# Kernel optimization log

Hardware: AMD Instinct MI355X
Metric: run time of the kernel (lower is better)

## Reference

```python
import jax, jax.numpy as jnp
import numpy as np

BN_EPS = 1e-3  # Keras BatchNormalization default epsilon
K = 7          # kernel_size


def setup_inputs() -> dict:
    key = jax.random.key(0)
    ks = jax.random.split(key, 5)
    B, L, C, F = 128, 512, 128, 128
    L_out = L - K + 1  # 506, valid padding, stride 1
    x = jax.random.normal(ks[0], (B, L, C), dtype=jnp.float32)
    # LocallyConnected1D unshared weights: (L_out, K*C, F), lecun_normal ~ N(0, 1/fan_in)
    kernel = jax.random.normal(ks[1], (L_out, K * C, F), dtype=jnp.float32) * (1.0 / np.sqrt(K * C))
    bias = jnp.zeros((L_out, F), dtype=jnp.float32)
    gamma = jnp.ones((F,), dtype=jnp.float32)
    beta = jnp.zeros((F,), dtype=jnp.float32)
    moving_mean = jax.random.normal(ks[2], (F,), dtype=jnp.float32) * 0.1
    moving_var = jax.random.uniform(ks[3], (F,), dtype=jnp.float32, minval=0.5, maxval=1.5)
    return {"x": x, "kernel": kernel, "bias": bias, "gamma": gamma,
            "beta": beta, "moving_mean": moving_mean, "moving_var": moving_var}


def _local_block(x, kernel, bias, gamma, beta, moving_mean, moving_var):
    B, L, C = x.shape
    L_out = L - K + 1
    F = kernel.shape[-1]
    # Patch extraction: idx[l, k] = l + k -> patches (B, L_out, K, C)
    idx = jnp.arange(L_out)[:, None] + jnp.arange(K)[None, :]
    patches = x[:, idx, :]                                  # (B, L_out, K, C)
    w = kernel.reshape(L_out, K, C, F)                      # unshared per-position weights
    y = jnp.einsum('blkc,lkcf->blf', patches, w) + bias     # (B, L_out, F)
    # BatchNorm (inference, axis=-1) fused with affine
    inv = gamma * jax.lax.rsqrt(moving_var + BN_EPS)
    y = y * inv + (beta - moving_mean * inv)
    return jax.nn.relu(y)


def reference(x, kernel, bias, gamma, beta, moving_mean, moving_var):
    return _local_block(x, kernel, bias, gamma, beta, moving_mean, moving_var)
```

## Files before the change

kernel.cpp:

```cpp
#include <hip/hip_runtime.h>
#include <hip/hip_bf16.h>

#define LO 506
#define LL 512
#define CC 128
#define FF 128
#define KC 896
#define BK 32
#define NK 28
#define XS 40
#define WS 40

typedef __attribute__((ext_vector_type(8))) short short8;
typedef __attribute__((ext_vector_type(4))) float floatx4;
typedef __attribute__((ext_vector_type(4))) unsigned int uintx4;
typedef unsigned short ushort_t;

static __device__ __forceinline__ unsigned int pk2(float a, float b) {
    __hip_bfloat16 ha = __float2bfloat16(a);
    __hip_bfloat16 hb = __float2bfloat16(b);
    unsigned short ua, ub;
    __builtin_memcpy(&ua, &ha, 2);
    __builtin_memcpy(&ub, &hb, 2);
    return (unsigned int)ua | ((unsigned int)ub << 16);
}

__global__ __launch_bounds__(512, 4)
void local_block_kernel(const float* __restrict__ x,
                        const float* __restrict__ wg,
                        const float* __restrict__ bias,
                        const float* __restrict__ gamma,
                        const float* __restrict__ beta,
                        const float* __restrict__ mmean,
                        const float* __restrict__ mvar,
                        float* __restrict__ out)
{
    const int bid = blockIdx.x;
    const int xcd = bid & 7;
    const int idx = bid >> 3;
    const int q8  = LO >> 3;
    const int r8  = LO & 7;
    const int l   = (xcd < r8) ? xcd * (q8 + 1) + idx
                               : r8 * (q8 + 1) + (xcd - r8) * q8 + idx;

    const int t    = threadIdx.x;
    const int lane = t & 63;
    const int wave = t >> 6;
    const int q    = lane >> 4;
    const int l16  = lane & 15;
    const int wr   = wave >> 1;
    const int wc   = wave & 1;

    __shared__ __align__(16) ushort_t Xs[2][128 * XS];
    __shared__ __align__(16) ushort_t Wt[2][128 * WS];

    const int am  = t >> 2;
    const int ak0 = (t & 3) * 8;
    const float* aptr = x + (size_t)am * (LL * CC) + l * CC + ak0;

    const int wf  = t & 127;
    const int wk  = (t >> 7) * 8;
    const float* wptr = wg + (size_t)l * (KC * FF) + wf;

    floatx4 acc[2][4] = {};

    floatx4 areg0[2], areg1[2];
    float   wreg0[8], wreg1[8];

#define LOAD_A(AR, KT) { const float* p = aptr + (KT) * BK;                     \
        AR[0] = *(const floatx4*)(p);                                           \
        AR[1] = *(const floatx4*)(p + 4); }

#define LOAD_W(WR, KT) { const float* p = wptr + (size_t)((KT) * BK + wk) * FF; \
        _Pragma("unroll") for (int j = 0; j < 8; ++j)                           \
            WR[j] = __builtin_nontemporal_load(p + j * FF); }

#define STAGE(S, AR, WR) {                                                      \
        uintx4 av = { pk2(AR[0].x, AR[0].y), pk2(AR[0].z, AR[0].w),             \
                      pk2(AR[1].x, AR[1].y), pk2(AR[1].z, AR[1].w) };           \
        *(uintx4*)&Xs[S][am * XS + ak0] = av;                                   \
        uintx4 wv = { pk2(WR[0], WR[1]), pk2(WR[2], WR[3]),                     \
                      pk2(WR[4], WR[5]), pk2(WR[6], WR[7]) };                   \
        *(uintx4*)&Wt[S][wf * WS + wk] = wv; }

#define BAR() {                                                                 \
        asm volatile("s_waitcnt lgkmcnt(0)" ::: "memory");                      \
        __builtin_amdgcn_s_barrier();                                           \
        asm volatile("" ::: "memory"); }

#define COMPUTE(S) {                                                            \
        short8 af[2], bfr[4];                                                   \
        _Pragma("unroll") for (int mi = 0; mi < 2; ++mi)                        \
            af[mi] = *(const short8*)&Xs[S][(wr*32 + mi*16 + l16) * XS + q*8];  \
        _Pragma("unroll") for (int ni = 0; ni < 4; ++ni)                        \
            bfr[ni] = *(const short8*)&Wt[S][(wc*64 + ni*16 + l16) * WS + q*8]; \
        _Pragma("unroll") for (int mi = 0; mi < 2; ++mi)                        \
            _Pragma("unroll") for (int ni = 0; ni < 4; ++ni)                    \
                acc[mi][ni] = __builtin_amdgcn_mfma_f32_16x16x32_bf16(          \
                    af[mi], bfr[ni], acc[mi][ni], 0, 0, 0); }

    LOAD_A(areg0, 0); LOAD_W(wreg0, 0);
    LOAD_A(areg1, 1); LOAD_W(wreg1, 1);

    for (int kt = 0; kt < NK; kt += 2) {
        STAGE(0, areg0, wreg0);
        if (kt + 2 < NK) { LOAD_A(areg0, kt + 2); LOAD_W(wreg0, kt + 2); }
        BAR();
        COMPUTE(0);
        STAGE(1, areg1, wreg1);
        if (kt + 3 < NK) { LOAD_A(areg1, kt + 3); LOAD_W(wreg1, kt + 3); }
        BAR();
        COMPUTE(1);
    }

#pragma unroll
    for (int ni = 0; ni < 4; ++ni) {
        int f = wc*64 + ni*16 + l16;
        float inv = gamma[f] * rsqrtf(mvar[f] + 1e-3f);
        float off = bias[l * FF + f] * inv + beta[f] - mmean[f] * inv;
#pragma unroll
        for (int mi = 0; mi < 2; ++mi) {
#pragma unroll
            for (int rg = 0; rg < 4; ++rg) {
                int b = wr*32 + mi*16 + q*4 + rg;
                float v = acc[mi][ni][rg] * inv + off;
                __builtin_nontemporal_store(fmaxf(v, 0.0f),
                    &out[((size_t)b * LO + l) * FF + f]);
            }
        }
    }
#undef LOAD_A
#undef LOAD_W
#undef STAGE
#undef BAR
#undef COMPUTE
}

extern "C" void kernel_launch(void* const* d_in, const int* in_sizes, int n_in,
                              void* d_out, int out_size, void* d_ws, size_t ws_size,
                              hipStream_t stream) {
    const float* x     = (const float*)d_in[0];
    const float* w     = (const float*)d_in[1];
    const float* bias  = (const float*)d_in[2];
    const float* gamma = (const float*)d_in[3];
    const float* beta  = (const float*)d_in[4];
    const float* mmean = (const float*)d_in[5];
    const float* mvar  = (const float*)d_in[6];
    float* out = (float*)d_out;

    local_block_kernel<<<dim3(LO), dim3(512), 0, stream>>>(
        x, w, bias, gamma, beta, mmean, mvar, out);
}
```

Before: 347.9 us.

## Split batch into two halves per position to double block count

Result: slower. 364.6 us (+4.8%).

```diff
diff --git a/kernel.cpp b/kernel.cpp
--- a/kernel.cpp
+++ b/kernel.cpp
@@ -8,12 +8,14 @@
 #define KC 896
 #define BK 32
 #define NK 28
+#define NB 1012
 #define XS 40
 #define WS 40
 
 typedef __attribute__((ext_vector_type(8))) short short8;
 typedef __attribute__((ext_vector_type(4))) float floatx4;
 typedef __attribute__((ext_vector_type(4))) unsigned int uintx4;
+typedef __attribute__((ext_vector_type(2))) unsigned int uintx2;
 typedef unsigned short ushort_t;
 
 static __device__ __forceinline__ unsigned int pk2(float a, float b) {
@@ -38,47 +40,46 @@
     const int bid = blockIdx.x;
     const int xcd = bid & 7;
     const int idx = bid >> 3;
-    const int q8  = LO >> 3;
-    const int r8  = LO & 7;
-    const int l   = (xcd < r8) ? xcd * (q8 + 1) + idx
+    const int q8  = NB >> 3;
+    const int r8  = NB & 7;
+    const int lin = (xcd < r8) ? xcd * (q8 + 1) + idx
                                : r8 * (q8 + 1) + (xcd - r8) * q8 + idx;
+    const int l     = lin >> 1;
+    const int bhalf = lin & 1;
 
     const int t    = threadIdx.x;
     const int lane = t & 63;
     const int wave = t >> 6;
     const int q    = lane >> 4;
     const int l16  = lane & 15;
-    const int wr   = wave >> 1;
-    const int wc   = wave & 1;
+    const int wrow = wave >> 2;
+    const int wcol = wave & 3;
 
-    __shared__ __align__(16) ushort_t Xs[2][128 * XS];
+    __shared__ __align__(16) ushort_t Xs[2][64 * XS];
     __shared__ __align__(16) ushort_t Wt[2][128 * WS];
 
-    const int am  = t >> 2;
-    const int ak0 = (t & 3) * 8;
-    const float* aptr = x + (size_t)am * (LL * CC) + l * CC + ak0;
+    const int am  = t >> 3;
+    const int ak0 = (t & 7) * 4;
+    const float* aptr = x + (size_t)(bhalf * 64 + am) * (LL * CC) + l * CC + ak0;
 
     const int wf  = t & 127;
     const int wk  = (t >> 7) * 8;
     const float* wptr = wg + (size_t)l * (KC * FF) + wf;
 
-    floatx4 acc[2][4] = {};
+    floatx4 acc[2][2] = {};
 
-    floatx4 areg0[2], areg1[2];
+    floatx4 areg0, areg1;
     float   wreg0[8], wreg1[8];
 
-#define LOAD_A(AR, KT) { const float* p = aptr + (KT) * BK;                     \
-        AR[0] = *(const floatx4*)(p);                                           \
-        AR[1] = *(const floatx4*)(p + 4); }
+#define LOAD_A(AR, KT) { AR = *(const floatx4*)(aptr + (KT) * BK); }
 
 #define LOAD_W(WR, KT) { const float* p = wptr + (size_t)((KT) * BK + wk) * FF; \
         _Pragma("unroll") for (int j = 0; j < 8; ++j)                           \
-            WR[j] = __builtin_nontemporal_load(p + j * FF); }
+            WR[j] = p[j * FF]; }
 
 #define STAGE(S, AR, WR) {                                                      \
-        uintx4 av = { pk2(AR[0].x, AR[0].y), pk2(AR[0].z, AR[0].w),             \
-                      pk2(AR[1].x, AR[1].y), pk2(AR[1].z, AR[1].w) };           \
-        *(uintx4*)&Xs[S][am * XS + ak0] = av;                                   \
+        uintx2 av = { pk2(AR.x, AR.y), pk2(AR.z, AR.w) };                       \
+        *(uintx2*)&Xs[S][am * XS + ak0] = av;                                   \
         uintx4 wv = { pk2(WR[0], WR[1]), pk2(WR[2], WR[3]),                     \
                       pk2(WR[4], WR[5]), pk2(WR[6], WR[7]) };                   \
         *(uintx4*)&Wt[S][wf * WS + wk] = wv; }
@@ -89,13 +90,13 @@
         asm volatile("" ::: "memory"); }
 
 #define COMPUTE(S) {                                                            \
-        short8 af[2], bfr[4];                                                   \
+        short8 af[2], bfr[2];                                                   \
         _Pragma("unroll") for (int mi = 0; mi < 2; ++mi)                        \
-            af[mi] = *(const short8*)&Xs[S][(wr*32 + mi*16 + l16) * XS + q*8];  \
-        _Pragma("unroll") for (int ni = 0; ni < 4; ++ni)                        \
-            bfr[ni] = *(const short8*)&Wt[S][(wc*64 + ni*16 + l16) * WS + q*8]; \
+            af[mi] = *(const short8*)&Xs[S][(wrow*32 + mi*16 + l16) * XS + q*8];\
+        _Pragma("unroll") for (int ni = 0; ni < 2; ++ni)                        \
+            bfr[ni] = *(const short8*)&Wt[S][(wcol*32 + ni*16 + l16) * WS + q*8];\
         _Pragma("unroll") for (int mi = 0; mi < 2; ++mi)                        \
-            _Pragma("unroll") for (int ni = 0; ni < 4; ++ni)                    \
+            _Pragma("unroll") for (int ni = 0; ni < 2; ++ni)                    \
                 acc[mi][ni] = __builtin_amdgcn_mfma_f32_16x16x32_bf16(          \
                     af[mi], bfr[ni], acc[mi][ni], 0, 0, 0); }
 
@@ -114,15 +115,15 @@
     }
 
 #pragma unroll
-    for (int ni = 0; ni < 4; ++ni) {
-        int f = wc*64 + ni*16 + l16;
+    for (int ni = 0; ni < 2; ++ni) {
+        int f = wcol*32 + ni*16 + l16;
         float inv = gamma[f] * rsqrtf(mvar[f] + 1e-3f);
         float off = bias[l * FF + f] * inv + beta[f] - mmean[f] * inv;
 #pragma unroll
         for (int mi = 0; mi < 2; ++mi) {
 #pragma unroll
             for (int rg = 0; rg < 4; ++rg) {
-                int b = wr*32 + mi*16 + q*4 + rg;
+                int b = bhalf*64 + wrow*32 + mi*16 + q*4 + rg;
                 float v = acc[mi][ni][rg] * inv + off;
                 __builtin_nontemporal_store(fmaxf(v, 0.0f),
                     &out[((size_t)b * LO + l) * FF + f]);
@@ -148,6 +149,6 @@
     const float* mvar  = (const float*)d_in[6];
     float* out = (float*)d_out;
 
-    local_block_kernel<<<dim3(LO), dim3(512), 0, stream>>>(
+    local_block_kernel<<<dim3(NB), dim3(512), 0, stream>>>(
         x, w, bias, gamma, beta, mmean, mvar, out);
 }
```
